# Performance work log

Measured on AMD Instinct MI355X. Metric: run time of the kernel, lower is better.

## Reference

```python
import jax, jax.numpy as jnp
import numpy as np

H = 64  # hidden size

def _lstm_last_hidden(x, W_ih, W_hh, b_ih, b_hh):
    # x: [B, T, I]; PyTorch gate order: i, f, g, o in stacked 4H rows.
    B, T, _ = x.shape
    # Precompute input projections for all timesteps: [T, B, 4H]
    x_proj = jnp.einsum('bti,gi->tbg', x, W_ih) + (b_ih + b_hh)

    def step(carry, xp):
        h, c = carry
        gates = xp + h @ W_hh.T  # [B, 4H]
        i = jax.nn.sigmoid(gates[:, 0*H:1*H])
        f = jax.nn.sigmoid(gates[:, 1*H:2*H])
        g = jnp.tanh(gates[:, 2*H:3*H])
        o = jax.nn.sigmoid(gates[:, 3*H:4*H])
        c = f * c + i * g
        h = o * jnp.tanh(c)
        return (h, c), None

    h0 = jnp.zeros((B, H), dtype=x.dtype)
    c0 = jnp.zeros((B, H), dtype=x.dtype)
    (h_last, _), _ = jax.lax.scan(step, (h0, c0), x_proj)
    return h_last

def setup_inputs() -> dict:
    key = jax.random.key(0)
    ks = jax.random.split(key, 7)
    B, T, I, C = 2048, 2048, 1, 3
    s = 1.0 / np.sqrt(H)  # PyTorch LSTM init scale
    return {
        'x': jax.random.normal(ks[0], (B, T, I), dtype=jnp.float32),
        'W_ih': jax.random.uniform(ks[1], (4*H, I), jnp.float32, -s, s),
        'W_hh': jax.random.uniform(ks[2], (4*H, H), jnp.float32, -s, s),
        'b_ih': jax.random.uniform(ks[3], (4*H,), jnp.float32, -s, s),
        'b_hh': jax.random.uniform(ks[4], (4*H,), jnp.float32, -s, s),
        'W_lin': jax.random.uniform(ks[5], (C, H), jnp.float32, -s, s),
        'b_lin': jax.random.uniform(ks[6], (C,), jnp.float32, -s, s),
    }

def reference(x, W_ih, W_hh, b_ih, b_hh, W_lin, b_lin):
    h_last = _lstm_last_hidden(x, W_ih, W_hh, b_ih, b_hh)  # [B, H]
    logits = h_last @ W_lin.T + b_lin                      # [B, C]
    return jax.nn.log_softmax(logits, axis=1)
```

## Files before the change

kernel.cpp:

```cpp
#include <hip/hip_runtime.h>
#include <hip/hip_bf16.h>

#define T_LEN 2048
#define HDIM  64
#define BT    4
#define XS    (T_LEN + 4)
#define HS    72
#define L2E   1.4426950408889634f
#define L2E2  2.8853900817779268f

typedef __attribute__((ext_vector_type(8))) short bf16x8;
typedef __attribute__((ext_vector_type(4))) float f32x4;

__device__ __forceinline__ float rcp_f(float x)  { return __builtin_amdgcn_rcpf(x); }
__device__ __forceinline__ float exp2_f(float x) { return __builtin_amdgcn_exp2f(x); }
__device__ __forceinline__ unsigned short f2bf(float f) {
    unsigned int u = __float_as_uint(f);
    u += 0x7fffu + ((u >> 16) & 1u);
    return (unsigned short)(u >> 16);
}

__global__ __launch_bounds__(256, 2) void lstm_mfma_kernel(
    const float* __restrict__ x,
    const float* __restrict__ W_ih,
    const float* __restrict__ W_hh,
    const float* __restrict__ b_ih,
    const float* __restrict__ b_hh,
    const float* __restrict__ W_lin,
    const float* __restrict__ b_lin,
    float* __restrict__ out)
{
    const int tid  = threadIdx.x;
    const int lane = tid & 63;
    const int wv   = tid >> 6;
    const int col  = lane & 15;
    const int hi   = lane >> 4;
    const int bq   = col & 3;
    const int s    = col >> 2;
    const int b0   = blockIdx.x * BT;

    __shared__ float sx[BT][XS];
    __shared__ short hl[2][BT][HS];
    __shared__ float red[BT][3];

    for (int i = tid; i < 2 * BT * HS; i += 256) ((short*)hl)[i] = 0;

    #pragma unroll
    for (int q = 0; q < 8; ++q) {
        const int idx = q * 256 + tid;
        const int row = idx >> 9;
        const int c4  = idx & 511;
        *(float4*)&sx[row][c4 * 4] =
            ((const float4*)(x + (size_t)(b0 + row) * T_LEN))[c4];
    }

    const float scl[4] = {L2E, L2E, L2E2, L2E};
    bf16x8 wf[4][2];
    #pragma unroll
    for (int g = 0; g < 4; ++g) {
        const int rowA = 64 * g + 16 * wv + col;
        #pragma unroll
        for (int kc = 0; kc < 2; ++kc) {
            const float* p = W_hh + rowA * HDIM + kc * 32 + hi * 8;
            bf16x8 f;
            #pragma unroll
            for (int j = 0; j < 8; ++j) f[j] = (short)f2bf(p[j] * scl[g]);
            wf[g][kc] = f;
        }
    }
    float wih1[4], bias1[4];
    #pragma unroll
    for (int g = 0; g < 4; ++g) {
        const int row = 64 * g + 16 * wv + hi * 4 + s;
        wih1[g]  = W_ih[row] * scl[g];
        bias1[g] = (b_ih[row] + b_hh[row]) * scl[g];
    }

    float cst = 0.f, hf = 0.f;
    const int sb0 = s & 1, sb1 = s >> 1;
    const int hwr = 16 * wv + hi * 4 + s;
    const int hi8 = hi * 8;

    const f32x4 zq = {0.f, 0.f, 0.f, 0.f};

    const short* hrd0 = &hl[0][bq][0];
    const short* hrd1 = &hl[1][bq][0];
    short* hwp1 = &hl[1][bq][hwr];
    short* hwp0 = &hl[0][bq][hwr];
    const float* xp = &sx[bq][0];

    __syncthreads();

#define STEP(HRD, HWP, XV) do {                                               \
    const bf16x8 hb0 = *(const bf16x8*)((HRD) + hi8);                         \
    const bf16x8 hb1 = *(const bf16x8*)((HRD) + 32 + hi8);                    \
    f32x4 a0 = __builtin_amdgcn_mfma_f32_16x16x32_bf16(wf[0][0], hb0, zq, 0, 0, 0); \
    f32x4 a1 = __builtin_amdgcn_mfma_f32_16x16x32_bf16(wf[1][0], hb0, zq, 0, 0, 0); \
    f32x4 a2 = __builtin_amdgcn_mfma_f32_16x16x32_bf16(wf[2][0], hb0, zq, 0, 0, 0); \
    f32x4 a3 = __builtin_amdgcn_mfma_f32_16x16x32_bf16(wf[3][0], hb0, zq, 0, 0, 0); \
    a0 = __builtin_amdgcn_mfma_f32_16x16x32_bf16(wf[0][1], hb1, a0, 0, 0, 0); \
    a1 = __builtin_amdgcn_mfma_f32_16x16x32_bf16(wf[1][1], hb1, a1, 0, 0, 0); \
    a2 = __builtin_amdgcn_mfma_f32_16x16x32_bf16(wf[2][1], hb1, a2, 0, 0, 0); \
    a3 = __builtin_amdgcn_mfma_f32_16x16x32_bf16(wf[3][1], hb1, a3, 0, 0, 0); \
    const float g0 = (sb1 ? (sb0 ? a0[3] : a0[2]) : (sb0 ? a0[1] : a0[0]))    \
                     + (bias1[0] + wih1[0] * (XV));                           \
    const float g1 = (sb1 ? (sb0 ? a1[3] : a1[2]) : (sb0 ? a1[1] : a1[0]))    \
                     + (bias1[1] + wih1[1] * (XV));                           \
    const float g2 = (sb1 ? (sb0 ? a2[3] : a2[2]) : (sb0 ? a2[1] : a2[0]))    \
                     + (bias1[2] + wih1[2] * (XV));                           \
    const float g3 = (sb1 ? (sb0 ? a3[3] : a3[2]) : (sb0 ? a3[1] : a3[0]))    \
                     + (bias1[3] + wih1[3] * (XV));                           \
    const float e0 = exp2_f(-g0);                                             \
    const float e1 = exp2_f(-g1);                                             \
    const float e2 = exp2_f(g2);                                              \
    const float e3 = exp2_f(-g3);                                             \
    const float fv = rcp_f(1.0f + e1);                                        \
    const float ig = (e2 - 1.0f) * rcp_f((1.0f + e0) * (e2 + 1.0f));          \
    cst = fv * cst + ig;                                                      \
    const float cc = fminf(cst, 32.0f);      \
    const float eC = exp2_f(L2E2 * cc);                                       \
    hf = (eC - 1.0f) * rcp_f((1.0f + e3) * (eC + 1.0f));                      \
    unsigned int rr;                                                          \
    asm("v_cvt_pk_bf16_f32 %0, %1, %1" : "=v"(rr) : "v"(hf));                 \
    *(HWP) = (short)rr;                                                       \
} while (0)

    for (int t = 0; t < T_LEN; t += 2) {
        const float2 xv2 = *(const float2*)(xp + t);
        STEP(hrd0, hwp1, xv2.x);
        __syncthreads();
        STEP(hrd1, hwp0, xv2.y);
        __syncthreads();
    }
#undef STEP

    float p0 = W_lin[0 * HDIM + hwr] * hf;
    float p1 = W_lin[1 * HDIM + hwr] * hf;
    float p2 = W_lin[2 * HDIM + hwr] * hf;
    #pragma unroll
    for (int m = 4; m <= 32; m <<= 1) {
        p0 += __shfl_xor(p0, m);
        p1 += __shfl_xor(p1, m);
        p2 += __shfl_xor(p2, m);
    }
    if (tid < BT * 3) ((float*)red)[tid] = 0.f;
    __syncthreads();
    if (lane < 4) {
        atomicAdd(&red[lane][0], p0);
        atomicAdd(&red[lane][1], p1);
        atomicAdd(&red[lane][2], p2);
    }
    __syncthreads();
    if (tid < BT) {
        const float l0 = red[tid][0] + b_lin[0];
        const float l1 = red[tid][1] + b_lin[1];
        const float l2 = red[tid][2] + b_lin[2];
        const float m  = fmaxf(l0, fmaxf(l1, l2));
        const float sm = __expf(l0 - m) + __expf(l1 - m) + __expf(l2 - m);
        const float ls = __logf(sm);
        out[(b0 + tid) * 3 + 0] = l0 - m - ls;
        out[(b0 + tid) * 3 + 1] = l1 - m - ls;
        out[(b0 + tid) * 3 + 2] = l2 - m - ls;
    }
}

extern "C" void kernel_launch(void* const* d_in, const int* in_sizes, int n_in,
                              void* d_out, int out_size, void* d_ws, size_t ws_size,
                              hipStream_t stream) {
    const float* x     = (const float*)d_in[0];
    const float* W_ih  = (const float*)d_in[1];
    const float* W_hh  = (const float*)d_in[2];
    const float* b_ih  = (const float*)d_in[3];
    const float* b_hh  = (const float*)d_in[4];
    const float* W_lin = (const float*)d_in[5];
    const float* b_lin = (const float*)d_in[6];
    float* out = (float*)d_out;

    const int B = in_sizes[0] / T_LEN;
    lstm_mfma_kernel<<<B / BT, 256, 0, stream>>>(x, W_ih, W_hh, b_ih, b_hh,
                                                 W_lin, b_lin, out);
}
```

Before: 528.9 us.

## Split LSTM gate work across two lane roles with 512-thread blocks

```diff
diff --git a/kernel.cpp b/kernel.cpp
--- a/kernel.cpp
+++ b/kernel.cpp
@@ -20,7 +20,7 @@
     return (unsigned short)(u >> 16);
 }
 
-__global__ __launch_bounds__(256, 2) void lstm_mfma_kernel(
+__global__ __launch_bounds__(512, 4) void lstm_mfma_kernel(
     const float* __restrict__ x,
     const float* __restrict__ W_ih,
     const float* __restrict__ W_hh,
@@ -30,63 +30,72 @@
     const float* __restrict__ b_lin,
     float* __restrict__ out)
 {
-    const int tid  = threadIdx.x;
-    const int lane = tid & 63;
-    const int wv   = tid >> 6;
-    const int col  = lane & 15;
-    const int hi   = lane >> 4;
-    const int bq   = col & 3;
-    const int s    = col >> 2;
-    const int b0   = blockIdx.x * BT;
+    const int tid    = threadIdx.x;
+    const int lane   = tid & 63;
+    const int wv     = tid >> 6;
+    const int col    = lane & 15;
+    const int hi     = lane >> 4;
+    const int bq     = col & 3;
+    const int s      = col >> 2;
+    const int r      = hi * 4 + s;
+    const int j      = r & 7;
+    const int roleHi = r >> 3;
+    const int unit   = 8 * wv + j;
+    const int b0     = blockIdx.x * BT;
 
     __shared__ float sx[BT][XS];
-    __shared__ short hl[2][BT][HS];
+    __shared__ short hl[2][2 * BT][HS];
     __shared__ float red[BT][3];
 
-    for (int i = tid; i < 2 * BT * HS; i += 256) ((short*)hl)[i] = 0;
+    for (int i = tid; i < 2 * 2 * BT * HS; i += 512) ((short*)hl)[i] = 0;
 
     #pragma unroll
-    for (int q = 0; q < 8; ++q) {
-        const int idx = q * 256 + tid;
+    for (int q = 0; q < 4; ++q) {
+        const int idx = q * 512 + tid;
         const int row = idx >> 9;
         const int c4  = idx & 511;
         *(float4*)&sx[row][c4 * 4] =
             ((const float4*)(x + (size_t)(b0 + row) * T_LEN))[c4];
     }
 
-    const float scl[4] = {L2E, L2E, L2E2, L2E};
-    bf16x8 wf[4][2];
-    #pragma unroll
-    for (int g = 0; g < 4; ++g) {
-        const int rowA = 64 * g + 16 * wv + col;
+    bf16x8 wf[2][2];
+    {
+        const int am = col;
         #pragma unroll
-        for (int kc = 0; kc < 2; ++kc) {
-            const float* p = W_hh + rowA * HDIM + kc * 32 + hi * 8;
-            bf16x8 f;
+        for (int tile = 0; tile < 2; ++tile) {
+            const int Wrow = (tile == 0)
+                ? ((am < 8) ? (8 * wv + am)       : (64  + 8 * wv + am - 8))
+                : ((am < 8) ? (128 + 8 * wv + am) : (192 + 8 * wv + am - 8));
+            const float sc = (tile == 1 && am < 8) ? L2E2 : -L2E;
             #pragma unroll
-            for (int j = 0; j < 8; ++j) f[j] = (short)f2bf(p[j] * scl[g]);
-            wf[g][kc] = f;
+            for (int kc = 0; kc < 2; ++kc) {
+                const float* p = W_hh + Wrow * HDIM + kc * 32 + hi * 8;
+                bf16x8 f;
+                #pragma unroll
+                for (int jj = 0; jj < 8; ++jj) f[jj] = (short)f2bf(p[jj] * sc);
+                wf[tile][kc] = f;
+            }
         }
     }
-    float wih1[4], bias1[4];
-    #pragma unroll
-    for (int g = 0; g < 4; ++g) {
-        const int row = 64 * g + 16 * wv + hi * 4 + s;
-        wih1[g]  = W_ih[row] * scl[g];
-        bias1[g] = (b_ih[row] + b_hh[row]) * scl[g];
-    }
+    const int   R0   = (roleHi ? 64 : 0) + unit;
+    const int   R1   = (roleHi ? 192 : 128) + unit;
+    const float s1   = roleHi ? -L2E : L2E2;
+    const float wih0 = W_ih[R0] * -L2E, bias0 = (b_ih[R0] + b_hh[R0]) * -L2E;
+    const float wih1 = W_ih[R1] * s1,   bias1 = (b_ih[R1] + b_hh[R1]) * s1;
+    const float A1c  = roleHi ? 1.0f : -2.0f;
+    const float B1c  = roleHi ? 0.0f : 1.0f;
 
-    float cst = 0.f, hf = 0.f;
+    float cY = 0.f, hf = 0.f;
     const int sb0 = s & 1, sb1 = s >> 1;
-    const int hwr = 16 * wv + hi * 4 + s;
     const int hi8 = hi * 8;
+    const int rowW = bq + (roleHi ? 0 : 4);
 
     const f32x4 zq = {0.f, 0.f, 0.f, 0.f};
 
     const short* hrd0 = &hl[0][bq][0];
     const short* hrd1 = &hl[1][bq][0];
-    short* hwp1 = &hl[1][bq][hwr];
-    short* hwp0 = &hl[0][bq][hwr];
+    short* hwp1 = &hl[1][rowW][unit];
+    short* hwp0 = &hl[0][rowW][unit];
     const float* xp = &sx[bq][0];
 
     __syncthreads();
@@ -96,30 +105,23 @@
     const bf16x8 hb1 = *(const bf16x8*)((HRD) + 32 + hi8);                    \
     f32x4 a0 = __builtin_amdgcn_mfma_f32_16x16x32_bf16(wf[0][0], hb0, zq, 0, 0, 0); \
     f32x4 a1 = __builtin_amdgcn_mfma_f32_16x16x32_bf16(wf[1][0], hb0, zq, 0, 0, 0); \
-    f32x4 a2 = __builtin_amdgcn_mfma_f32_16x16x32_bf16(wf[2][0], hb0, zq, 0, 0, 0); \
-    f32x4 a3 = __builtin_amdgcn_mfma_f32_16x16x32_bf16(wf[3][0], hb0, zq, 0, 0, 0); \
     a0 = __builtin_amdgcn_mfma_f32_16x16x32_bf16(wf[0][1], hb1, a0, 0, 0, 0); \
     a1 = __builtin_amdgcn_mfma_f32_16x16x32_bf16(wf[1][1], hb1, a1, 0, 0, 0); \
-    a2 = __builtin_amdgcn_mfma_f32_16x16x32_bf16(wf[2][1], hb1, a2, 0, 0, 0); \
-    a3 = __builtin_amdgcn_mfma_f32_16x16x32_bf16(wf[3][1], hb1, a3, 0, 0, 0); \
-    const float g0 = (sb1 ? (sb0 ? a0[3] : a0[2]) : (sb0 ? a0[1] : a0[0]))    \
-                     + (bias1[0] + wih1[0] * (XV));                           \
-    const float g1 = (sb1 ? (sb0 ? a1[3] : a1[2]) : (sb0 ? a1[1] : a1[0]))    \
-                     + (bias1[1] + wih1[1] * (XV));                           \
-    const float g2 = (sb1 ? (sb0 ? a2[3] : a2[2]) : (sb0 ? a2[1] : a2[0]))    \
-                     + (bias1[2] + wih1[2] * (XV));                           \
-    const float g3 = (sb1 ? (sb0 ? a3[3] : a3[2]) : (sb0 ? a3[1] : a3[0]))    \
-                     + (bias1[3] + wih1[3] * (XV));                           \
-    const float e0 = exp2_f(-g0);                                             \
-    const float e1 = exp2_f(-g1);                                             \
-    const float e2 = exp2_f(g2);                                              \
-    const float e3 = exp2_f(-g3);                                             \
-    const float fv = rcp_f(1.0f + e1);                                        \
-    const float ig = (e2 - 1.0f) * rcp_f((1.0f + e0) * (e2 + 1.0f));          \
-    cst = fv * cst + ig;                                                      \
-    const float cc = fminf(cst, 32.0f);      \
-    const float eC = exp2_f(L2E2 * cc);                                       \
-    hf = (eC - 1.0f) * rcp_f((1.0f + e3) * (eC + 1.0f));                      \
+    const float sel0 = sb1 ? (sb0 ? a0[3] : a0[2]) : (sb0 ? a0[1] : a0[0]);   \
+    const float sel1 = sb1 ? (sb0 ? a1[3] : a1[2]) : (sb0 ? a1[1] : a1[0]);   \
+    const float y0 = sel0 + (bias0 + wih0 * (XV));                            \
+    const float y1 = sel1 + (bias1 + wih1 * (XV));                            \
+    const float e0 = exp2_f(y0);                                              \
+    const float e1 = exp2_f(y1);                                              \
+    const float v0 = rcp_f(1.0f + e0);               \
+    const float v1 = A1c * rcp_f(1.0f + e1) + B1c;    \
+    const float ps = v0 * v1;                       \
+    const float pr = __shfl_xor(ps, 32);                                      \
+    cY = v0 * cY + pr * L2E2;                          \
+    const float yc = fminf(cY, 92.0f);                  \
+    const float e2 = exp2_f(yc);                                              \
+    const float th = 1.0f - 2.0f * rcp_f(1.0f + e2);                          \
+    hf = v1 * th;                                   \
     unsigned int rr;                                                          \
     asm("v_cvt_pk_bf16_f32 %0, %1, %1" : "=v"(rr) : "v"(hf));                 \
     *(HWP) = (short)rr;                                                       \
@@ -134,14 +136,15 @@
     }
 #undef STEP
 
-    float p0 = W_lin[0 * HDIM + hwr] * hf;
-    float p1 = W_lin[1 * HDIM + hwr] * hf;
-    float p2 = W_lin[2 * HDIM + hwr] * hf;
+    const float hfM = roleHi ? hf : 0.0f;
+    float p0 = W_lin[0 * HDIM + unit] * hfM;
+    float p1 = W_lin[1 * HDIM + unit] * hfM;
+    float p2 = W_lin[2 * HDIM + unit] * hfM;
     #pragma unroll
-    for (int m = 4; m <= 32; m <<= 1) {
-        p0 += __shfl_xor(p0, m);
-        p1 += __shfl_xor(p1, m);
-        p2 += __shfl_xor(p2, m);
+    for (int mm = 4; mm <= 32; mm <<= 1) {
+        p0 += __shfl_xor(p0, mm);
+        p1 += __shfl_xor(p1, mm);
+        p2 += __shfl_xor(p2, mm);
     }
     if (tid < BT * 3) ((float*)red)[tid] = 0.f;
     __syncthreads();
@@ -177,6 +180,6 @@
     float* out = (float*)d_out;
 
     const int B = in_sizes[0] / T_LEN;
-    lstm_mfma_kernel<<<B / BT, 256, 0, stream>>>(x, W_ih, W_hh, b_ih, b_hh,
+    lstm_mfma_kernel<<<B / BT, 512, 0, stream>>>(x, W_ih, W_hh, b_ih, b_hh,
                                                  W_lin, b_lin, out);
 }
```

New measurement: 752.8 us. 1.42x slower.
